# Optimization experiments

Measured on AMD Instinct MI355X. Metric: run time of the kernel, lower is better.

The kernel has to match this reference:

```python
import jax, jax.numpy as jnp
import numpy as np

B, N, C, H = 4, 1024, 768, 12
D = C // H
HID = 4 * C
SCALE = D ** -0.5
EPS = 1e-6


def layernorm(x, w, b):
    mu = jnp.mean(x, axis=-1, keepdims=True)
    var = jnp.mean(jnp.square(x - mu), axis=-1, keepdims=True)
    return (x - mu) * jax.lax.rsqrt(var + EPS) * w + b


def setup_inputs() -> dict:
    key = jax.random.key(0)
    ks = jax.random.split(key, 16)
    s = lambda fan_in: 1.0 / np.sqrt(fan_in)
    return {
        "x": jax.random.normal(ks[0], (B, N, C), jnp.float32),
        "physics_bias": jax.random.normal(ks[1], (B, N, N), jnp.float32),
        "qkv_w": jax.random.normal(ks[2], (C, 3 * C), jnp.float32) * s(C),
        "qkv_b": jnp.zeros((3 * C,), jnp.float32),
        "proj_w": jax.random.normal(ks[3], (C, C), jnp.float32) * s(C),
        "proj_b": jnp.zeros((C,), jnp.float32),
        "n1_w": jnp.ones((C,), jnp.float32),
        "n1_b": jnp.zeros((C,), jnp.float32),
        "n2_w": jnp.ones((C,), jnp.float32),
        "n2_b": jnp.zeros((C,), jnp.float32),
        "fc1_w": jax.random.normal(ks[4], (C, HID), jnp.float32) * s(C),
        "fc1_b": jnp.zeros((HID,), jnp.float32),
        "fc2_w": jax.random.normal(ks[5], (HID, C), jnp.float32) * s(HID),
        "fc2_b": jnp.zeros((C,), jnp.float32),
    }


def reference(x, physics_bias, qkv_w, qkv_b, proj_w, proj_b,
              n1_w, n1_b, n2_w, n2_b, fc1_w, fc1_b, fc2_w, fc2_b):
    # --- biased self-attention (pre-norm) ---
    h = layernorm(x, n1_w, n1_b)                         # [B,N,C]
    qkv = (h @ qkv_w + qkv_b).reshape(B, N, 3, H, D)     # [B,N,3,H,D]
    q, k, v = (qkv[:, :, i] for i in range(3))           # each [B,N,H,D]
    attn = jnp.einsum('bnhd,bmhd->bhnm', q, k) * SCALE   # [B,H,N,N]
    attn = attn + physics_bias[:, None, :, :]            # additive physics bias
    attn = jax.nn.softmax(attn, axis=-1)
    o = jnp.einsum('bhnm,bmhd->bnhd', attn, v).reshape(B, N, C)
    x = x + (o @ proj_w + proj_b)
    # --- MLP (pre-norm) ---
    h = layernorm(x, n2_w, n2_b)
    h = jax.nn.gelu(h @ fc1_w + fc1_b, approximate=False)
    x = x + (h @ fc2_w + fc2_b)
    return x
```

## Files before the change

kernel.cpp:

```cpp
#include <hip/hip_runtime.h>
#include <hip/hip_bf16.h>
#include <cstdint>
#include <cstddef>

#define B_   4
#define N_   1024
#define C_   768
#define H_   12
#define D_   64
#define HID_ 3072
#define M_   4096

typedef __attribute__((ext_vector_type(8))) short short8;
typedef __attribute__((ext_vector_type(8))) unsigned short ushort8;
typedef __attribute__((ext_vector_type(4))) float f32x4;

__device__ __forceinline__ void gload16(const void* g, void* l) {
  __builtin_amdgcn_global_load_lds(
      (const __attribute__((address_space(1))) void*)g,
      (__attribute__((address_space(3))) void*)l, 16, 0, 0);
}

__device__ __forceinline__ unsigned short f2bf(float f) {
  __hip_bfloat16 h = __float2bfloat16(f);
  return __builtin_bit_cast(unsigned short, h);
}
__device__ __forceinline__ float bf2f(unsigned short u) {
  unsigned int x = ((unsigned int)u) << 16;
  return __builtin_bit_cast(float, x);
}
__device__ __forceinline__ float ex2(float x) {
  float r;
  asm("v_exp_f32 %0, %1" : "=v"(r) : "v"(x));
  return r;
}
__device__ __forceinline__ float frcp(float x) {
  float r;
  asm("v_rcp_f32 %0, %1" : "=v"(r) : "v"(x));
  return r;
}

__global__ __launch_bounds__(256) void wconv_all(
    const float* __restrict__ qkv_w, const float* __restrict__ proj_w,
    const float* __restrict__ fc1_w, const float* __restrict__ fc2_w,
    unsigned short* __restrict__ wt_qkv, unsigned short* __restrict__ wt_proj,
    unsigned short* __restrict__ wt_fc1, unsigned short* __restrict__ wt_fc2) {
  __shared__ float tile[32][33];
  const int bid = blockIdx.x;
  const float* W;
  unsigned short* Wt;
  int K, Nn, bx, by;
  if (bid < 1728) {
    W = qkv_w; Wt = wt_qkv; K = 768; Nn = 2304;
    bx = bid % 72; by = bid / 72;
  } else if (bid < 1728 + 576) {
    const int i = bid - 1728;
    W = proj_w; Wt = wt_proj; K = 768; Nn = 768;
    bx = i % 24; by = i / 24;
  } else if (bid < 1728 + 576 + 2304) {
    const int i = bid - (1728 + 576);
    W = fc1_w; Wt = wt_fc1; K = 768; Nn = 3072;
    bx = i % 96; by = i / 96;
  } else {
    const int i = bid - (1728 + 576 + 2304);
    W = fc2_w; Wt = wt_fc2; K = 3072; Nn = 768;
    bx = i % 24; by = i / 24;
  }
  const int tx = threadIdx.x & 31, ty = threadIdx.x >> 5;
  const int n0 = bx * 32, k0 = by * 32;
#pragma unroll
  for (int i = 0; i < 32; i += 8)
    tile[ty + i][tx] = W[(size_t)(k0 + ty + i) * Nn + n0 + tx];
  __syncthreads();
#pragma unroll
  for (int i = 0; i < 32; i += 8)
    Wt[(size_t)(n0 + ty + i) * K + k0 + tx] = f2bf(tile[tx][ty + i]);
}

__global__ __launch_bounds__(256) void ln_kernel(const float* __restrict__ x,
                                                 const float* __restrict__ w,
                                                 const float* __restrict__ b,
                                                 unsigned short* __restrict__ out) {
  __shared__ float sbuf[8];
  const int row = blockIdx.x;
  const int t = threadIdx.x;
  const float* xr = x + (size_t)row * C_;
  float v0 = xr[t], v1 = xr[t + 256], v2 = xr[t + 512];
  float s = v0 + v1 + v2;
  float ss = v0 * v0 + v1 * v1 + v2 * v2;
#pragma unroll
  for (int m = 32; m >= 1; m >>= 1) {
    s += __shfl_xor(s, m);
    ss += __shfl_xor(ss, m);
  }
  const int wave = t >> 6, lane = t & 63;
  if (lane == 0) { sbuf[wave] = s; sbuf[4 + wave] = ss; }
  __syncthreads();
  s = sbuf[0] + sbuf[1] + sbuf[2] + sbuf[3];
  ss = sbuf[4] + sbuf[5] + sbuf[6] + sbuf[7];
  const float mu = s * (1.f / C_);
  const float var = ss * (1.f / C_) - mu * mu;
  const float rstd = rsqrtf(var + 1e-6f);
  unsigned short* o = out + (size_t)row * C_;
  o[t]       = f2bf((v0 - mu) * rstd * w[t]       + b[t]);
  o[t + 256] = f2bf((v1 - mu) * rstd * w[t + 256] + b[t + 256]);
  o[t + 512] = f2bf((v2 - mu) * rstd * w[t + 512] + b[t + 512]);
}

template <bool GELU, bool RES, bool OUTF, bool OUTB>
__global__ __launch_bounds__(256) void gemm_bt(const unsigned short* __restrict__ A,
                                               const unsigned short* __restrict__ Bt,
                                               const float* __restrict__ bias,
                                               const float* __restrict__ res,
                                               float* __restrict__ outF,
                                               unsigned short* __restrict__ outB,
                                               int M, int Nn, int K) {
  __shared__ unsigned short As[5][128 * 32];
  __shared__ unsigned short Bs[5][128 * 32];
  const int t = threadIdx.x;
  const int lane = t & 63;
  const int wave = t >> 6;
  const int wm = wave >> 1, wn = wave & 1;
  const int r15 = lane & 15, g = lane >> 4;

  const int orig = blockIdx.y * 32 + blockIdx.x;
  const int xcd = orig & 7;
  const int j = orig >> 3;
  const int bm = xcd * 4 + (j & 3);
  const int bn = j >> 2;

  f32x4 acc[4][4];
#pragma unroll
  for (int m = 0; m < 4; ++m)
#pragma unroll
    for (int n = 0; n < 4; ++n) acc[m][n] = (f32x4){0.f, 0.f, 0.f, 0.f};

  const unsigned short* ga0 = A + (size_t)(bm * 128 + (t >> 2)) * K + (t & 3) * 8;
  const unsigned short* gb0 = Bt + (size_t)(bn * 128 + (t >> 2)) * K + (t & 3) * 8;

#define GSTAGE(kt_, buf_)                                                \
  {                                                                      \
    const unsigned short* ga = ga0 + (kt_)*32;                           \
    const unsigned short* gb = gb0 + (kt_)*32;                           \
    gload16(ga, (char*)As[buf_] + wave * 1024);                          \
    gload16(ga + (size_t)64 * K, (char*)As[buf_] + wave * 1024 + 4096);  \
    gload16(gb, (char*)Bs[buf_] + wave * 1024);                          \
    gload16(gb + (size_t)64 * K, (char*)Bs[buf_] + wave * 1024 + 4096);  \
  }

  const int nk = K >> 5;
  GSTAGE(0, 0);
  GSTAGE(1, 1);
  GSTAGE(2, 2);
  GSTAGE(3, 3);

  int rd = 0;
  for (int kt = 0; kt < nk; ++kt) {
    const int rem = nk - kt;
    if (rem >= 4)
      asm volatile("s_waitcnt vmcnt(12)" ::: "memory");
    else if (rem == 3)
      asm volatile("s_waitcnt vmcnt(8)" ::: "memory");
    else if (rem == 2)
      asm volatile("s_waitcnt vmcnt(4)" ::: "memory");
    else
      asm volatile("s_waitcnt vmcnt(0)" ::: "memory");
    __builtin_amdgcn_s_barrier();

    short8 af[4], bf[4];
#pragma unroll
    for (int m = 0; m < 4; ++m)
      af[m] = *(const short8*)(As[rd] + (wm * 64 + m * 16 + r15) * 32 + g * 8);
#pragma unroll
    for (int n = 0; n < 4; ++n)
      bf[n] = *(const short8*)(Bs[rd] + (wn * 64 + n * 16 + r15) * 32 + g * 8);

    if (kt + 4 < nk) {
      const int wr = (rd == 0) ? 4 : rd - 1;
      GSTAGE(kt + 4, wr);
    }

    asm volatile("s_waitcnt lgkmcnt(0)" ::: "memory");
    __builtin_amdgcn_sched_barrier(0);
    __builtin_amdgcn_s_setprio(1);
#pragma unroll
    for (int m = 0; m < 4; ++m)
#pragma unroll
      for (int n = 0; n < 4; ++n)
        acc[m][n] = __builtin_amdgcn_mfma_f32_16x16x32_bf16(af[m], bf[n], acc[m][n], 0, 0, 0);
    __builtin_amdgcn_s_setprio(0);
    rd = (rd == 4) ? 0 : rd + 1;
  }
#undef GSTAGE

#pragma unroll
  for (int m = 0; m < 4; ++m) {
#pragma unroll
    for (int n = 0; n < 4; ++n) {
#pragma unroll
      for (int r = 0; r < 4; ++r) {
        const int row = bm * 128 + wm * 64 + m * 16 + g * 4 + r;
        const int col = bn * 128 + wn * 64 + n * 16 + r15;
        float v = acc[m][n][r] + bias[col];
        if (GELU) v = 0.5f * v * (1.f + erff(v * 0.70710678118654752f));
        if (RES) v += res[(size_t)row * Nn + col];
        if (OUTF) outF[(size_t)row * Nn + col] = v;
        if (OUTB) outB[(size_t)row * Nn + col] = f2bf(v);
      }
    }
  }
}

__global__ __launch_bounds__(256) void attn_kernel(const unsigned short* __restrict__ qkv,
                                                   const float* __restrict__ pbias,
                                                   unsigned short* __restrict__ o) {
  __shared__ unsigned short Ks[2][64 * 64];
  __shared__ unsigned short Vt[64 * 64];
  __shared__ unsigned short Ps[4][16 * 64];
  const int t = threadIdx.x, lane = t & 63, wave = t >> 6;
  const int bh = blockIdx.y;
  const int b = bh / H_, h = bh % H_;
  const int q0 = blockIdx.x * 64;
  const int r15 = lane & 15, g = lane >> 4;
  const int qrow = q0 + wave * 16;
  const float LOG2E = 1.44269504088896f;
  const float QS = 0.125f * 1.44269504088896f;
  const int NT = N_ / 64;

  short8 aq[2];
  {
    const unsigned short* qp =
        qkv + (size_t)(b * N_ + qrow + r15) * (3 * C_) + h * D_ + g * 8;
    const ushort8 r0 = *(const ushort8*)qp;
    const ushort8 r1 = *(const ushort8*)(qp + 32);
#pragma unroll
    for (int j = 0; j < 8; ++j) {
      aq[0][j] = (short)f2bf(bf2f(r0[j]) * QS);
      aq[1][j] = (short)f2bf(bf2f(r1[j]) * QS);
    }
  }

  f32x4 oacc[4];
#pragma unroll
  for (int n = 0; n < 4; ++n) oacc[n] = (f32x4){0.f, 0.f, 0.f, 0.f};
  float m_run[4], l_run[4];
#pragma unroll
  for (int r = 0; r < 4; ++r) { m_run[r] = -1e30f; l_run[r] = 0.f; }

  const unsigned short* kbase = qkv + (size_t)b * N_ * (3 * C_) + C_ + h * D_;
  const unsigned short* vbase = qkv + (size_t)b * N_ * (3 * C_) + 2 * C_ + h * D_;
  const float* bb = pbias + (size_t)b * N_ * N_;

  const int krow = t >> 3;
  const int kchunk = (t & 7) ^ (krow & 7);
  const int vp = t & 31;
  const int vq = t >> 5;
  const int vkey = vp * 2, vd0 = vq * 8;

#define KSTAGE(kb_, nb_)                                                       \
  {                                                                            \
    const unsigned short* kg =                                                 \
        kbase + (size_t)((kb_)*64 + krow) * (3 * C_) + kchunk * 8;             \
    gload16(kg, (char*)Ks[nb_] + wave * 1024);                                 \
    gload16(kg + (size_t)32 * (3 * C_), (char*)Ks[nb_] + wave * 1024 + 4096);  \
  }

#define VWRITE(va_, vb_)                                                             \
  {                                                                                  \
    char* vdst = (char*)Vt;                                                          \
    _Pragma("unroll") for (int jj = 0; jj < 8; ++jj) {                               \
      const int d = vd0 + jj;                                                        \
      const unsigned int pack =                                                      \
          (unsigned int)(va_)[jj] | ((unsigned int)(vb_)[jj] << 16);                 \
      *(unsigned int*)(vdst + d * 128 + (((vp >> 2) ^ (d & 7)) << 4) +               \
                       (vp & 3) * 4) = pack;                                         \
    }                                                                                \
  }

  KSTAGE(0, 0);
  ushort8 va, vb2;
  {
    const unsigned short* vg = vbase + (size_t)vkey * (3 * C_) + vd0;
    va = *(const ushort8*)vg;
    vb2 = *(const ushort8*)(vg + 3 * C_);
  }
  float bcur[4][4], bnext[4][4];
#pragma unroll
  for (int n = 0; n < 4; ++n)
#pragma unroll
    for (int r = 0; r < 4; ++r)
      bcur[n][r] = bb[(size_t)(qrow + g * 4 + r) * N_ + n * 16 + r15];

  for (int kb = 0; kb < NT; ++kb) {
    const int cur = kb & 1;
    __syncthreads();

    VWRITE(va, vb2);

    const bool more = (kb + 1 < NT);
    if (more) {
      KSTAGE(kb + 1, cur ^ 1);
      const unsigned short* vg =
          vbase + (size_t)((kb + 1) * 64 + vkey) * (3 * C_) + vd0;
      va = *(const ushort8*)vg;
      vb2 = *(const ushort8*)(vg + 3 * C_);
#pragma unroll
      for (int n = 0; n < 4; ++n)
#pragma unroll
        for (int r = 0; r < 4; ++r)
          bnext[n][r] =
              bb[(size_t)(qrow + g * 4 + r) * N_ + (kb + 1) * 64 + n * 16 + r15];
    }

    const unsigned short* Ksc = Ks[cur];
    f32x4 sacc[4];
#pragma unroll
    for (int n = 0; n < 4; ++n) sacc[n] = (f32x4){0.f, 0.f, 0.f, 0.f};
    __builtin_amdgcn_s_setprio(1);
#pragma unroll
    for (int kk = 0; kk < 2; ++kk) {
#pragma unroll
      for (int n = 0; n < 4; ++n) {
        short8 bk = *(const short8*)(Ksc + (n * 16 + r15) * 64 +
                                     (((kk * 4 + g) ^ (r15 & 7)) << 3));
        sacc[n] = __builtin_amdgcn_mfma_f32_16x16x32_bf16(aq[kk], bk, sacc[n], 0, 0, 0);
      }
    }
    __builtin_amdgcn_s_setprio(0);

    float p[4][4], tm[4];
#pragma unroll
    for (int r = 0; r < 4; ++r) tm[r] = -3e38f;
#pragma unroll
    for (int n = 0; n < 4; ++n)
#pragma unroll
      for (int r = 0; r < 4; ++r) {
        const float s = fmaf(bcur[n][r], LOG2E, sacc[n][r]);
        p[n][r] = s;
        tm[r] = fmaxf(tm[r], s);
      }
#pragma unroll
    for (int r = 0; r < 4; ++r) {
      tm[r] = fmaxf(tm[r], __shfl_xor(tm[r], 1));
      tm[r] = fmaxf(tm[r], __shfl_xor(tm[r], 2));
      tm[r] = fmaxf(tm[r], __shfl_xor(tm[r], 4));
      tm[r] = fmaxf(tm[r], __shfl_xor(tm[r], 8));
    }
    int need = 0;
#pragma unroll
    for (int r = 0; r < 4; ++r) need |= (tm[r] > m_run[r] + 8.0f);
    if (__any(need)) {
#pragma unroll
      for (int r = 0; r < 4; ++r) {
        const float mn = fmaxf(m_run[r], tm[r]);
        const float corr = ex2(m_run[r] - mn);
        m_run[r] = mn;
        l_run[r] *= corr;
#pragma unroll
        for (int n = 0; n < 4; ++n) oacc[n][r] *= corr;
      }
    }
    float rs[4] = {0.f, 0.f, 0.f, 0.f};
#pragma unroll
    for (int n = 0; n < 4; ++n)
#pragma unroll
      for (int r = 0; r < 4; ++r) {
        p[n][r] = ex2(p[n][r] - m_run[r]);
        rs[r] += p[n][r];
      }
#pragma unroll
    for (int r = 0; r < 4; ++r) {
      rs[r] += __shfl_xor(rs[r], 1);
      rs[r] += __shfl_xor(rs[r], 2);
      rs[r] += __shfl_xor(rs[r], 4);
      rs[r] += __shfl_xor(rs[r], 8);
      l_run[r] += rs[r];
    }

    unsigned short* Psw = Ps[wave];
#pragma unroll
    for (int n = 0; n < 4; ++n)
#pragma unroll
      for (int r = 0; r < 4; ++r) {
        const int row = g * 4 + r, col = n * 16 + r15;
        Psw[row * 64 + (((col >> 3) ^ (row & 7)) << 3) + (col & 7)] = f2bf(p[n][r]);
      }

    asm volatile("s_waitcnt lgkmcnt(0)" ::: "memory");
    __builtin_amdgcn_s_barrier();
    __builtin_amdgcn_sched_barrier(0);

    __builtin_amdgcn_s_setprio(1);
#pragma unroll
    for (int kk = 0; kk < 2; ++kk) {
      short8 ap = *(const short8*)(Psw + r15 * 64 + (((kk * 4 + g) ^ (r15 & 7)) << 3));
#pragma unroll
      for (int n = 0; n < 4; ++n) {
        short8 bv = *(const short8*)(Vt + (n * 16 + r15) * 64 +
                                     (((kk * 4 + g) ^ (r15 & 7)) << 3));
        oacc[n] = __builtin_amdgcn_mfma_f32_16x16x32_bf16(ap, bv, oacc[n], 0, 0, 0);
      }
    }
    __builtin_amdgcn_s_setprio(0);

    if (more) {
#pragma unroll
      for (int n = 0; n < 4; ++n)
#pragma unroll
        for (int r = 0; r < 4; ++r) bcur[n][r] = bnext[n][r];
    }
  }
#undef KSTAGE
#undef VWRITE

  float rl[4];
#pragma unroll
  for (int r = 0; r < 4; ++r) rl[r] = frcp(l_run[r]);
#pragma unroll
  for (int n = 0; n < 4; ++n) {
#pragma unroll
    for (int r = 0; r < 4; ++r) {
      const int row = qrow + g * 4 + r;
      const float v = oacc[n][r] * rl[r];
      o[(size_t)(b * N_ + row) * C_ + h * D_ + n * 16 + r15] = f2bf(v);
    }
  }
}

extern "C" void kernel_launch(void* const* d_in, const int* in_sizes, int n_in,
                              void* d_out, int out_size, void* d_ws, size_t ws_size,
                              hipStream_t stream) {
  const float* x      = (const float*)d_in[0];
  const float* pbias  = (const float*)d_in[1];
  const float* qkv_w  = (const float*)d_in[2];
  const float* qkv_b  = (const float*)d_in[3];
  const float* proj_w = (const float*)d_in[4];
  const float* proj_b = (const float*)d_in[5];
  const float* n1_w   = (const float*)d_in[6];
  const float* n1_b   = (const float*)d_in[7];
  const float* n2_w   = (const float*)d_in[8];
  const float* n2_b   = (const float*)d_in[9];
  const float* fc1_w  = (const float*)d_in[10];
  const float* fc1_b  = (const float*)d_in[11];
  const float* fc2_w  = (const float*)d_in[12];
  const float* fc2_b  = (const float*)d_in[13];
  float* out = (float*)d_out;

  char* ws = (char*)d_ws;
  unsigned short* wt_qkv  = (unsigned short*)(ws + 0);
  unsigned short* wt_proj = (unsigned short*)(ws + 3538944);
  unsigned short* wt_fc1  = (unsigned short*)(ws + 4718592);
  unsigned short* wt_fc2  = (unsigned short*)(ws + 9437184);
  float*          x2      = (float*)(ws + 14155776);
  unsigned short* h1      = (unsigned short*)(ws + 26738688);
  unsigned short* qkvb    = (unsigned short*)(ws + 33030144);

  wconv_all<<<1728 + 576 + 2304 + 2304, 256, 0, stream>>>(
      qkv_w, proj_w, fc1_w, fc2_w, wt_qkv, wt_proj, wt_fc1, wt_fc2);

  ln_kernel<<<M_, 256, 0, stream>>>(x, n1_w, n1_b, h1);
  gemm_bt<false, false, false, true><<<dim3(32, 18), 256, 0, stream>>>(
      h1, wt_qkv, qkv_b, nullptr, nullptr, qkvb, M_, 3 * C_, C_);
  attn_kernel<<<dim3(N_ / 64, B_ * H_), 256, 0, stream>>>(qkvb, pbias, h1);
  gemm_bt<false, true, true, false><<<dim3(32, 6), 256, 0, stream>>>(
      h1, wt_proj, proj_b, x, x2, nullptr, M_, C_, C_);
  ln_kernel<<<M_, 256, 0, stream>>>(x2, n2_w, n2_b, h1);
  gemm_bt<true, false, false, true><<<dim3(32, 24), 256, 0, stream>>>(
      h1, wt_fc1, fc1_b, nullptr, nullptr, qkvb, M_, HID_, C_);
  gemm_bt<false, true, true, false><<<dim3(32, 6), 256, 0, stream>>>(
      qkvb, wt_fc2, fc2_b, x2, out, nullptr, M_, C_, HID_);
}
```

Measured before the change: 214.0 us.

## Split attention KV range in two with log-sum-exp combine; halve M tile for narrow GEMMs

```diff
diff --git a/kernel.cpp b/kernel.cpp
--- a/kernel.cpp
+++ b/kernel.cpp
@@ -32,6 +32,11 @@
 __device__ __forceinline__ float ex2(float x) {
   float r;
   asm("v_exp_f32 %0, %1" : "=v"(r) : "v"(x));
+  return r;
+}
+__device__ __forceinline__ float lg2(float x) {
+  float r;
+  asm("v_log_f32 %0, %1" : "=v"(r) : "v"(x));
   return r;
 }
 __device__ __forceinline__ float frcp(float x) {
@@ -107,7 +112,7 @@
   o[t + 512] = f2bf((v2 - mu) * rstd * w[t + 512] + b[t + 512]);
 }
 
-template <bool GELU, bool RES, bool OUTF, bool OUTB>
+template <int MF, bool GELU, bool RES, bool OUTF, bool OUTB>
 __global__ __launch_bounds__(256) void gemm_bt(const unsigned short* __restrict__ A,
                                                const unsigned short* __restrict__ Bt,
                                                const float* __restrict__ bias,
@@ -115,7 +120,7 @@
                                                float* __restrict__ outF,
                                                unsigned short* __restrict__ outB,
                                                int M, int Nn, int K) {
-  __shared__ unsigned short As[5][128 * 32];
+  __shared__ unsigned short As[5][MF * 32 * 32];
   __shared__ unsigned short Bs[5][128 * 32];
   const int t = threadIdx.x;
   const int lane = t & 63;
@@ -123,29 +128,32 @@
   const int wm = wave >> 1, wn = wave & 1;
   const int r15 = lane & 15, g = lane >> 4;
 
-  const int orig = blockIdx.y * 32 + blockIdx.x;
+  constexpr int SPX = (MF == 4) ? 4 : 8;
+  constexpr int LGS = (MF == 4) ? 2 : 3;
+  const int orig = blockIdx.y * gridDim.x + blockIdx.x;
   const int xcd = orig & 7;
   const int j = orig >> 3;
-  const int bm = xcd * 4 + (j & 3);
-  const int bn = j >> 2;
-
-  f32x4 acc[4][4];
-#pragma unroll
-  for (int m = 0; m < 4; ++m)
+  const int bm = xcd * SPX + (j & (SPX - 1));
+  const int bn = j >> LGS;
+
+  f32x4 acc[MF][4];
+#pragma unroll
+  for (int m = 0; m < MF; ++m)
 #pragma unroll
     for (int n = 0; n < 4; ++n) acc[m][n] = (f32x4){0.f, 0.f, 0.f, 0.f};
 
-  const unsigned short* ga0 = A + (size_t)(bm * 128 + (t >> 2)) * K + (t & 3) * 8;
+  const unsigned short* ga0 = A + (size_t)(bm * (MF * 32) + (t >> 2)) * K + (t & 3) * 8;
   const unsigned short* gb0 = Bt + (size_t)(bn * 128 + (t >> 2)) * K + (t & 3) * 8;
 
-#define GSTAGE(kt_, buf_)                                                \
-  {                                                                      \
-    const unsigned short* ga = ga0 + (kt_)*32;                           \
-    const unsigned short* gb = gb0 + (kt_)*32;                           \
-    gload16(ga, (char*)As[buf_] + wave * 1024);                          \
-    gload16(ga + (size_t)64 * K, (char*)As[buf_] + wave * 1024 + 4096);  \
-    gload16(gb, (char*)Bs[buf_] + wave * 1024);                          \
-    gload16(gb + (size_t)64 * K, (char*)Bs[buf_] + wave * 1024 + 4096);  \
+#define GSTAGE(kt_, buf_)                                                  \
+  {                                                                        \
+    const unsigned short* ga = ga0 + (kt_)*32;                             \
+    const unsigned short* gb = gb0 + (kt_)*32;                             \
+    gload16(ga, (char*)As[buf_] + wave * 1024);                            \
+    if constexpr (MF == 4)                                                 \
+      gload16(ga + (size_t)64 * K, (char*)As[buf_] + wave * 1024 + 4096);  \
+    gload16(gb, (char*)Bs[buf_] + wave * 1024);                            \
+    gload16(gb + (size_t)64 * K, (char*)Bs[buf_] + wave * 1024 + 4096);    \
   }
 
   const int nk = K >> 5;
@@ -157,20 +165,24 @@
   int rd = 0;
   for (int kt = 0; kt < nk; ++kt) {
     const int rem = nk - kt;
-    if (rem >= 4)
-      asm volatile("s_waitcnt vmcnt(12)" ::: "memory");
-    else if (rem == 3)
-      asm volatile("s_waitcnt vmcnt(8)" ::: "memory");
-    else if (rem == 2)
-      asm volatile("s_waitcnt vmcnt(4)" ::: "memory");
-    else
+    if (rem >= 4) {
+      if constexpr (MF == 4) asm volatile("s_waitcnt vmcnt(12)" ::: "memory");
+      else                   asm volatile("s_waitcnt vmcnt(9)" ::: "memory");
+    } else if (rem == 3) {
+      if constexpr (MF == 4) asm volatile("s_waitcnt vmcnt(8)" ::: "memory");
+      else                   asm volatile("s_waitcnt vmcnt(6)" ::: "memory");
+    } else if (rem == 2) {
+      if constexpr (MF == 4) asm volatile("s_waitcnt vmcnt(4)" ::: "memory");
+      else                   asm volatile("s_waitcnt vmcnt(3)" ::: "memory");
+    } else {
       asm volatile("s_waitcnt vmcnt(0)" ::: "memory");
+    }
     __builtin_amdgcn_s_barrier();
 
-    short8 af[4], bf[4];
-#pragma unroll
-    for (int m = 0; m < 4; ++m)
-      af[m] = *(const short8*)(As[rd] + (wm * 64 + m * 16 + r15) * 32 + g * 8);
+    short8 af[MF], bf[4];
+#pragma unroll
+    for (int m = 0; m < MF; ++m)
+      af[m] = *(const short8*)(As[rd] + (wm * (MF * 16) + m * 16 + r15) * 32 + g * 8);
 #pragma unroll
     for (int n = 0; n < 4; ++n)
       bf[n] = *(const short8*)(Bs[rd] + (wn * 64 + n * 16 + r15) * 32 + g * 8);
@@ -184,7 +196,7 @@
     __builtin_amdgcn_sched_barrier(0);
     __builtin_amdgcn_s_setprio(1);
 #pragma unroll
-    for (int m = 0; m < 4; ++m)
+    for (int m = 0; m < MF; ++m)
 #pragma unroll
       for (int n = 0; n < 4; ++n)
         acc[m][n] = __builtin_amdgcn_mfma_f32_16x16x32_bf16(af[m], bf[n], acc[m][n], 0, 0, 0);
@@ -194,12 +206,12 @@
 #undef GSTAGE
 
 #pragma unroll
-  for (int m = 0; m < 4; ++m) {
+  for (int m = 0; m < MF; ++m) {
 #pragma unroll
     for (int n = 0; n < 4; ++n) {
 #pragma unroll
       for (int r = 0; r < 4; ++r) {
-        const int row = bm * 128 + wm * 64 + m * 16 + g * 4 + r;
+        const int row = bm * (MF * 32) + wm * (MF * 16) + m * 16 + g * 4 + r;
         const int col = bn * 128 + wn * 64 + n * 16 + r15;
         float v = acc[m][n][r] + bias[col];
         if (GELU) v = 0.5f * v * (1.f + erff(v * 0.70710678118654752f));
@@ -213,7 +225,9 @@
 
 __global__ __launch_bounds__(256) void attn_kernel(const unsigned short* __restrict__ qkv,
                                                    const float* __restrict__ pbias,
-                                                   unsigned short* __restrict__ o) {
+                                                   unsigned short* __restrict__ On0,
+                                                   unsigned short* __restrict__ On1,
+                                                   float* __restrict__ sbuf) {
   __shared__ unsigned short Ks[2][64 * 64];
   __shared__ unsigned short Vt[64 * 64];
   __shared__ unsigned short Ps[4][16 * 64];
@@ -221,11 +235,12 @@
   const int bh = blockIdx.y;
   const int b = bh / H_, h = bh % H_;
   const int q0 = blockIdx.x * 64;
+  const int z = blockIdx.z;
+  const int kt0 = z * 8;
   const int r15 = lane & 15, g = lane >> 4;
   const int qrow = q0 + wave * 16;
   const float LOG2E = 1.44269504088896f;
   const float QS = 0.125f * 1.44269504088896f;
-  const int NT = N_ / 64;
 
   short8 aq[2];
   {
@@ -234,9 +249,9 @@
     const ushort8 r0 = *(const ushort8*)qp;
     const ushort8 r1 = *(const ushort8*)(qp + 32);
 #pragma unroll
-    for (int j = 0; j < 8; ++j) {
-      aq[0][j] = (short)f2bf(bf2f(r0[j]) * QS);
-      aq[1][j] = (short)f2bf(bf2f(r1[j]) * QS);
+    for (int jj = 0; jj < 8; ++jj) {
+      aq[0][jj] = (short)f2bf(bf2f(r0[jj]) * QS);
+      aq[1][jj] = (short)f2bf(bf2f(r1[jj]) * QS);
     }
   }
 
@@ -257,10 +272,10 @@
   const int vq = t >> 5;
   const int vkey = vp * 2, vd0 = vq * 8;
 
-#define KSTAGE(kb_, nb_)                                                       \
+#define KSTAGE(kt_, nb_)                                                       \
   {                                                                            \
     const unsigned short* kg =                                                 \
-        kbase + (size_t)((kb_)*64 + krow) * (3 * C_) + kchunk * 8;             \
+        kbase + (size_t)((kt_)*64 + krow) * (3 * C_) + kchunk * 8;             \
     gload16(kg, (char*)Ks[nb_] + wave * 1024);                                 \
     gload16(kg + (size_t)32 * (3 * C_), (char*)Ks[nb_] + wave * 1024 + 4096);  \
   }
@@ -277,10 +292,10 @@
     }                                                                                \
   }
 
-  KSTAGE(0, 0);
+  KSTAGE(kt0, 0);
   ushort8 va, vb2;
   {
-    const unsigned short* vg = vbase + (size_t)vkey * (3 * C_) + vd0;
+    const unsigned short* vg = vbase + (size_t)(kt0 * 64 + vkey) * (3 * C_) + vd0;
     va = *(const ushort8*)vg;
     vb2 = *(const ushort8*)(vg + 3 * C_);
   }
@@ -289,19 +304,20 @@
   for (int n = 0; n < 4; ++n)
 #pragma unroll
     for (int r = 0; r < 4; ++r)
-      bcur[n][r] = bb[(size_t)(qrow + g * 4 + r) * N_ + n * 16 + r15];
-
-  for (int kb = 0; kb < NT; ++kb) {
+      bcur[n][r] = bb[(size_t)(qrow + g * 4 + r) * N_ + kt0 * 64 + n * 16 + r15];
+
+  for (int kb = 0; kb < 8; ++kb) {
+    const int kt = kt0 + kb;
     const int cur = kb & 1;
     __syncthreads();
 
     VWRITE(va, vb2);
 
-    const bool more = (kb + 1 < NT);
+    const bool more = (kb + 1 < 8);
     if (more) {
-      KSTAGE(kb + 1, cur ^ 1);
+      KSTAGE(kt + 1, cur ^ 1);
       const unsigned short* vg =
-          vbase + (size_t)((kb + 1) * 64 + vkey) * (3 * C_) + vd0;
+          vbase + (size_t)((kt + 1) * 64 + vkey) * (3 * C_) + vd0;
       va = *(const ushort8*)vg;
       vb2 = *(const ushort8*)(vg + 3 * C_);
 #pragma unroll
@@ -309,7 +325,7 @@
 #pragma unroll
         for (int r = 0; r < 4; ++r)
           bnext[n][r] =
-              bb[(size_t)(qrow + g * 4 + r) * N_ + (kb + 1) * 64 + n * 16 + r15];
+              bb[(size_t)(qrow + g * 4 + r) * N_ + (kt + 1) * 64 + n * 16 + r15];
     }
 
     const unsigned short* Ksc = Ks[cur];
@@ -413,6 +429,7 @@
 #undef KSTAGE
 #undef VWRITE
 
+  unsigned short* On = z ? On1 : On0;
   float rl[4];
 #pragma unroll
   for (int r = 0; r < 4; ++r) rl[r] = frcp(l_run[r]);
@@ -422,9 +439,40 @@
     for (int r = 0; r < 4; ++r) {
       const int row = qrow + g * 4 + r;
       const float v = oacc[n][r] * rl[r];
-      o[(size_t)(b * N_ + row) * C_ + h * D_ + n * 16 + r15] = f2bf(v);
-    }
-  }
+      On[(size_t)(b * N_ + row) * C_ + h * D_ + n * 16 + r15] = f2bf(v);
+    }
+  }
+  if (r15 == 0) {
+#pragma unroll
+    for (int r = 0; r < 4; ++r) {
+      const int row = qrow + g * 4 + r;
+      sbuf[((size_t)(z * B_ + b) * H_ + h) * N_ + row] = m_run[r] + lg2(l_run[r]);
+    }
+  }
+}
+
+__global__ __launch_bounds__(256) void attn_combine(
+    const unsigned short* __restrict__ On0, const unsigned short* __restrict__ On1,
+    const float* __restrict__ sbuf, unsigned short* __restrict__ o) {
+  const int tid = blockIdx.x * 256 + threadIdx.x;
+  const size_t base = (size_t)tid * 8;
+  const int row = (int)(base / C_);
+  const int c = (int)(base % C_);
+  const int b = row >> 10;
+  const int h = c >> 6;
+  const size_t sidx = ((size_t)(b * H_ + h)) * N_ + (row & 1023);
+  const float s0 = sbuf[sidx];
+  const float s1 = sbuf[(size_t)B_ * H_ * N_ + sidx];
+  const float smax = fmaxf(s0, s1);
+  const float w0 = ex2(s0 - smax), w1 = ex2(s1 - smax);
+  const float inv = frcp(w0 + w1);
+  const ushort8 a0 = *(const ushort8*)(On0 + base);
+  const ushort8 a1 = *(const ushort8*)(On1 + base);
+  ushort8 r;
+#pragma unroll
+  for (int jj = 0; jj < 8; ++jj)
+    r[jj] = f2bf((w0 * bf2f(a0[jj]) + w1 * bf2f(a1[jj])) * inv);
+  *(ushort8*)(o + base) = r;
 }
 
 extern "C" void kernel_launch(void* const* d_in, const int* in_sizes, int n_in,
@@ -452,21 +500,25 @@
   unsigned short* wt_fc1  = (unsigned short*)(ws + 4718592);
   unsigned short* wt_fc2  = (unsigned short*)(ws + 9437184);
   float*          x2      = (float*)(ws + 14155776);
+  unsigned short* On1     = (unsigned short*)(ws + 14155776);
   unsigned short* h1      = (unsigned short*)(ws + 26738688);
   unsigned short* qkvb    = (unsigned short*)(ws + 33030144);
+  unsigned short* On0     = (unsigned short*)(ws + 51904512);
+  float*          sb      = (float*)(ws + 58195968);
 
   wconv_all<<<1728 + 576 + 2304 + 2304, 256, 0, stream>>>(
       qkv_w, proj_w, fc1_w, fc2_w, wt_qkv, wt_proj, wt_fc1, wt_fc2);
 
   ln_kernel<<<M_, 256, 0, stream>>>(x, n1_w, n1_b, h1);
-  gemm_bt<false, false, false, true><<<dim3(32, 18), 256, 0, stream>>>(
+  gemm_bt<4, false, false, false, true><<<dim3(32, 18), 256, 0, stream>>>(
       h1, wt_qkv, qkv_b, nullptr, nullptr, qkvb, M_, 3 * C_, C_);
-  attn_kernel<<<dim3(N_ / 64, B_ * H_), 256, 0, stream>>>(qkvb, pbias, h1);
-  gemm_bt<false, true, true, false><<<dim3(32, 6), 256, 0, stream>>>(
+  attn_kernel<<<dim3(N_ / 64, B_ * H_, 2), 256, 0, stream>>>(qkvb, pbias, On0, On1, sb);
+  attn_combine<<<(M_ * C_) / (256 * 8), 256, 0, stream>>>(On0, On1, sb, h1);
+  gemm_bt<2, false, true, true, false><<<dim3(64, 6), 256, 0, stream>>>(
       h1, wt_proj, proj_b, x, x2, nullptr, M_, C_, C_);
   ln_kernel<<<M_, 256, 0, stream>>>(x2, n2_w, n2_b, h1);
-  gemm_bt<true, false, false, true><<<dim3(32, 24), 256, 0, stream>>>(
+  gemm_bt<4, true, false, false, true><<<dim3(32, 24), 256, 0, stream>>>(
       h1, wt_fc1, fc1_b, nullptr, nullptr, qkvb, M_, HID_, C_);
-  gemm_bt<false, true, true, false><<<dim3(32, 6), 256, 0, stream>>>(
+  gemm_bt<2, false, true, true, false><<<dim3(64, 6), 256, 0, stream>>>(
       qkvb, wt_fc2, fc2_b, x2, out, nullptr, M_, C_, HID_);
 }
```

After: 220.2 us. +2.9%, slower.
